# Kernel optimization log

Measured on AMD Instinct MI355X. Metric: run time of the kernel, lower is better.

Reference implementation:

```python
import jax, jax.numpy as jnp
import numpy as np

N_ATOMS = 10000
N_PAIRS = 320000
C = 64        # channel width (pp_nodes[-1], ii_nodes[-1], pi_nodes[-1])
NB = 10       # n_basis
EPS = 1e-3    # torsion-boost epsilon


def setup_inputs() -> dict:
    key = jax.random.key(0)
    ks = jax.random.split(key, 24)
    f32 = jnp.float32

    def w(k, shp):
        return jax.random.normal(k, shp, f32) / np.float32(np.sqrt(shp[0]))

    ind_2 = jax.random.randint(ks[0], (N_PAIRS, 2), 0, N_ATOMS)
    p1 = jax.random.normal(ks[1], (N_ATOMS, C), f32)
    p3 = jax.random.normal(ks[2], (N_ATOMS, 3, C), f32)
    basis = jax.random.uniform(ks[3], (N_PAIRS, NB), dtype=f32)
    d3 = jax.random.normal(ks[4], (N_PAIRS, 3), f32)
    d3 = d3 / jnp.linalg.norm(d3, axis=-1, keepdims=True)  # unit bond directions
    fc_edge = jax.random.uniform(ks[5], (N_PAIRS, 1), dtype=f32)  # cutoff in [0,1]

    return {
        'ind_2': ind_2, 'p1': p1, 'p3': p3, 'basis': basis, 'd3': d3, 'fc_edge': fc_edge,
        'pp_pre_W1': w(ks[6], (C, C)), 'pp_pre_b1': jnp.zeros((C,), f32),
        'pp_pre_W2': w(ks[7], (C, C)), 'pp_pre_b2': jnp.zeros((C,), f32),
        'pi_W': w(ks[8], (2 * C, C * NB)), 'pi_b': jnp.zeros((C * NB,), f32),
        'ii_W': w(ks[9], (C, 2 * C)),
        'pp_post_W1': w(ks[10], (2 * C, C)), 'pp_post_W2': w(ks[11], (C, C)),
        'eq_pp_W': w(ks[12], (C, C)),
        'pp1_W1': w(ks[13], (2 * C, C)), 'pp1_b1': jnp.zeros((C,), f32),
        'pp1_W2': w(ks[14], (C, 2 * C)), 'pp1_b2': jnp.zeros((2 * C,), f32),
    }


def _gc_block(ind_2, p1, p3, basis, d3, fc_edge,
              pp_pre_W1, pp_pre_b1, pp_pre_W2, pp_pre_b2,
              pi_W, pi_b, ii_W, pp_post_W1, pp_post_W2,
              eq_pp_W, pp1_W1, pp1_b1, pp1_W2, pp1_b2):
    n_atoms = p1.shape[0]
    i = ind_2[:, 0]
    j = ind_2[:, 1]

    # ---- InvarLayer ----
    # pp_pre: FF [C,C], tanh, bias
    p1_in = jnp.tanh(jnp.tanh(p1 @ pp_pre_W1 + pp_pre_b1) @ pp_pre_W2 + pp_pre_b2)
    # PILayer: concat(p1[i], p1[j]) -> Dense(C*NB) -> contract with radial basis
    pair = jnp.concatenate([p1_in[i], p1_in[j]], axis=-1)            # (P, 2C)
    h = jnp.tanh(pair @ pi_W + pi_b).reshape(-1, C, NB)              # (P, C, NB)
    i_pair = jnp.einsum('pcb,pb->pc', h, basis)                      # (P, C)
    # ii: FF [2C] (doubled for n_props=2), tanh, no bias
    i_pair = jnp.tanh(i_pair @ ii_W)                                 # (P, 2C)
    # IP: scatter-add onto receiver atom i
    p1_scat = jax.ops.segment_sum(i_pair, i, num_segments=n_atoms)   # (N, 2C)
    # pp_post: FF [C,C], tanh, no bias
    p1_new = jnp.tanh(jnp.tanh(p1_scat @ pp_post_W1) @ pp_post_W2)   # (N, C)

    i1a, i1b = jnp.split(i_pair, 2, axis=-1)  # chunks; rank-3 branch uses i1s[1]

    # ---- torsion boost (compute_torsion_boost_t3) ----
    v = jax.ops.segment_sum(d3 * fc_edge, i, num_segments=n_atoms)   # (N, 3)
    v_i = v[i]
    proj = jnp.sum(v_i * d3, axis=-1, keepdims=True)
    w = v_i - proj * d3                                              # perpendicular part
    w2 = jnp.sum(w * w, axis=-1, keepdims=True)
    g_deg = w2 / (w2 + (10.0 * EPS) ** 2)
    t3 = w * jax.lax.rsqrt(w2 + EPS * EPS) * g_deg                   # (P, 3)
    tb_gate = g_deg * (fc_edge * fc_edge)                            # (P, 1)

    # ---- EquivarLayer ----
    gate = i1b[:, None, :]                                           # (P, 1, C)
    ix = p3[j] * gate + d3[:, :, None] * gate \
         + t3[:, :, None] * (i1b * tb_gate)[:, None, :]              # (P, 3, C)
    p3_new = jax.ops.segment_sum(ix, i, num_segments=n_atoms)        # (N, 3, C)
    p3_new = p3_new @ eq_pp_W                                        # PP: no bias, no act
    dotted = jnp.einsum('ixr,ixr->ir', p3_new, p3_new)               # (N, C)

    # ---- output PP + gating ----
    h2 = jnp.tanh(jnp.concatenate([p1_new, dotted], axis=-1) @ pp1_W1 + pp1_b1)
    h2 = jnp.tanh(h2 @ pp1_W2 + pp1_b2)                              # (N, 2C)
    g1, g3 = jnp.split(h2, 2, axis=-1)
    p1_out = g1                                                      # (N, C)
    p3_out = p3_new * g3[:, None, :]                                 # ScaleLayer
    return p1_out, p3_out


def reference(ind_2, p1, p3, basis, d3, fc_edge,
              pp_pre_W1, pp_pre_b1, pp_pre_W2, pp_pre_b2,
              pi_W, pi_b, ii_W, pp_post_W1, pp_post_W2,
              eq_pp_W, pp1_W1, pp1_b1, pp1_W2, pp1_b2):
    return _gc_block(ind_2, p1, p3, basis, d3, fc_edge,
                     pp_pre_W1, pp_pre_b1, pp_pre_W2, pp_pre_b2,
                     pi_W, pi_b, ii_W, pp_post_W1, pp_post_W2,
                     eq_pp_W, pp1_W1, pp1_b1, pp1_W2, pp1_b2)
```

## Files before the change

kernel.cpp:

```cpp
#include <hip/hip_runtime.h>
#include <hip/hip_bf16.h>

#define N_ATOMS 10000
#define N_PAIRS 320000
#define C_ 64
#define NB_ 10

typedef short bf16x8 __attribute__((ext_vector_type(8)));
typedef float f32x4 __attribute__((ext_vector_type(4)));

__device__ __forceinline__ float bf2f(__hip_bfloat16 x) { return __bfloat162float(x); }
__device__ __forceinline__ float ldf(const void* p, int i, int isf32) {
    return isf32 ? ((const float*)p)[i] : bf2f(((const __hip_bfloat16*)p)[i]);
}
__device__ __forceinline__ short f2bs(float x) {
    __hip_bfloat16 h = __float2bfloat16(x);
    return *reinterpret_cast<short*>(&h);
}
__device__ __forceinline__ float bs2f(unsigned short s) {
    return __uint_as_float(((unsigned)s) << 16);
}
__device__ __forceinline__ float tanh_fast(float x) {
    const float e = __expf(2.0f * x);
    return 1.0f - 2.0f * __builtin_amdgcn_rcpf(e + 1.0f);
}

#define W_PPREW1 0
#define W_PPREB1 4096
#define W_PPREW2 4160
#define W_PPREB2 8256
#define W_PIW    8320
#define W_PIB    90240
#define W_IIW    90880
#define W_PPOSTW1 99072
#define W_PPOSTW2 107264
#define W_EQW    111360
#define W_Q1W    115456
#define W_Q1B    123648
#define W_Q2W    123712
#define W_Q2B    131904
#define W_TOTAL  132032

__device__ __forceinline__ int probe_eval(const void* d3)
{
    float sf = 0.f, sb = 0.f;
    const float* f = (const float*)d3;
    const __hip_bfloat16* b = (const __hip_bfloat16*)d3;
    for (int r = 0; r < 4; r++) {
        float x = f[r*3], y = f[r*3+1], z = f[r*3+2];
        float n = x*x + y*y + z*z;
        sf += isfinite(n) ? fabsf(n - 1.f) : 1e30f;
        float xb = bf2f(b[r*3]), yb = bf2f(b[r*3+1]), zb = bf2f(b[r*3+2]);
        float nb = xb*xb + yb*yb + zb*zb;
        sb += isfinite(nb) ? fabsf(nb - 1.f) : 1e30f;
    }
    return (sf < sb) ? 1 : 0;
}

__global__ __launch_bounds__(256) void k_front(
    const void* __restrict__ d3, const void* __restrict__ fc,
    int* __restrict__ flag, const int* __restrict__ ind2,
    int* __restrict__ cnt, float* __restrict__ v,
    const void* s0, const void* s1, const void* s2, const void* s3,
    const void* s4, const void* s5, const void* s6, const void* s7,
    const void* s8, const void* s9, const void* s10, const void* s11,
    const void* s12, const void* s13,
    float* __restrict__ wbuf)
{
    __shared__ int fsh;
    if (threadIdx.x == 0) {
        const int fv = probe_eval(d3);
        fsh = fv;
        if (blockIdx.x == 0) *flag = fv;
    }
    __syncthreads();
    const int isf32 = fsh;
    if (blockIdx.x < 1250) {
        const int p = blockIdx.x * 256 + threadIdx.x;
        if (p >= N_PAIRS) return;
        const int ia = ind2[2 * p];
        atomicAdd(&cnt[ia], 1);
        const float f = ldf(fc, p, isf32);
        #pragma unroll
        for (int x = 0; x < 3; x++)
            atomicAdd(&v[ia * 3 + x], ldf(d3, 3 * p + x, isf32) * f);
        return;
    }
    const int idx = (blockIdx.x - 1250) * 256 + threadIdx.x;
    if (idx >= W_TOTAL) return;
    const int offw[15] = {W_PPREW1, W_PPREB1, W_PPREW2, W_PPREB2, W_PIW, W_PIB,
                          W_IIW, W_PPOSTW1, W_PPOSTW2, W_EQW, W_Q1W, W_Q1B,
                          W_Q2W, W_Q2B, W_TOTAL};
    const void* srcs[14] = {s0,s1,s2,s3,s4,s5,s6,s7,s8,s9,s10,s11,s12,s13};
    int t = 0;
    while (idx >= offw[t + 1]) t++;
    wbuf[idx] = ldf(srcs[t], idx - offw[t], isf32);
}

__global__ __launch_bounds__(256) void k_scan_wfrag(
    const int* __restrict__ cnt, int* __restrict__ offs, int* __restrict__ cur,
    const float* __restrict__ wbuf,
    short* __restrict__ w1Fh, short* __restrict__ w1Fl,
    short* __restrict__ w2Fh, short* __restrict__ w2Fl,
    short* __restrict__ pAh, short* __restrict__ pAl,
    short* __restrict__ pBh, short* __restrict__ pBl,
    short* __restrict__ pEh, short* __restrict__ pEl,
    short* __restrict__ pQ1h, short* __restrict__ pQ1l,
    short* __restrict__ pQ2h, short* __restrict__ pQ2l)
{
    const int b = blockIdx.x;
    if (b == 0) {
        if (!cnt) return;
        __shared__ int part[256];
        __shared__ int base[257];
        const int t = threadIdx.x;
        const int lo = t * 40, hi = (lo + 40 < N_ATOMS) ? lo + 40 : N_ATOMS;
        int s = 0;
        for (int bb = lo; bb < hi; bb++) s += cnt[bb];
        part[t] = s;
        __syncthreads();
        if (t == 0) {
            int run = 0;
            for (int i = 0; i < 256; i++) { base[i] = run; run += part[i]; }
            base[256] = run;
        }
        __syncthreads();
        int run = base[t];
        for (int bb = lo; bb < hi; bb++) { offs[bb] = run; cur[bb] = run; run += cnt[bb]; }
        if (t == 0) offs[N_ATOMS] = base[256];
        return;
    }
    if (b < 33) {
        const int bb = b - 1;
        const int isW2 = bb >= 16;
        const int idx = (bb - (isW2 ? 16 : 0)) * 256 + threadIdx.x;
        const int j = idx & 7, lane = (idx >> 3) & 63, s2 = (idx >> 9) & 1, ct = idx >> 10;
        const int k = s2 * 32 + (lane >> 4) * 8 + j;
        const int col = ct * 16 + (lane & 15);
        const float wv = wbuf[(isW2 ? W_PPREW2 : W_PPREW1) + k * 64 + col];
        const short hs = f2bs(wv);
        short* dh = isW2 ? w2Fh : w1Fh;
        short* dl = isW2 ? w2Fl : w1Fl;
        dh[idx] = hs;
        dl[idx] = f2bs(wv - bs2f((unsigned short)hs));
        return;
    }
    if (b < 65 || (b >= 97 && b < 129)) {
        const int isQ1 = (b >= 97);
        const int idx = (b - (isQ1 ? 97 : 33)) * 256 + threadIdx.x;
        const int j = idx & 7, lane = (idx >> 3) & 63, s = (idx >> 9) & 3, tt = idx >> 11;
        const int k = s * 32 + (lane >> 4) * 8 + j;
        const int col = tt * 16 + (lane & 15);
        const float wv = wbuf[(isQ1 ? W_Q1W : W_PPOSTW1) + k * 64 + col];
        const short hs = f2bs(wv);
        short* dh = isQ1 ? pQ1h : pAh;
        short* dl = isQ1 ? pQ1l : pAl;
        dh[idx] = hs;
        dl[idx] = f2bs(wv - bs2f((unsigned short)hs));
        return;
    }
    if (b < 97) {
        const int isE = b >= 81;
        const int idx = (b - (isE ? 81 : 65)) * 256 + threadIdx.x;
        const int j = idx & 7, lane = (idx >> 3) & 63, s2 = (idx >> 9) & 1, ct = idx >> 10;
        const int k = s2 * 32 + (lane >> 4) * 8 + j;
        const int col = ct * 16 + (lane & 15);
        const float wv = wbuf[(isE ? W_EQW : W_PPOSTW2) + k * 64 + col];
        const short hs = f2bs(wv);
        short* dh = isE ? pEh : pBh;
        short* dl = isE ? pEl : pBl;
        dh[idx] = hs;
        dl[idx] = f2bs(wv - bs2f((unsigned short)hs));
        return;
    }
    {
        const int idx = (b - 129) * 256 + threadIdx.x;
        const int j = idx & 7, lane = (idx >> 3) & 63, s2 = (idx >> 9) & 1, ct = idx >> 10;
        const int k = s2 * 32 + (lane >> 4) * 8 + j;
        const int col = ct * 16 + (lane & 15);
        const float wv = wbuf[W_Q2W + k * 128 + col];
        const short hs = f2bs(wv);
        pQ2h[idx] = hs;
        pQ2l[idx] = f2bs(wv - bs2f((unsigned short)hs));
    }
}

__global__ __launch_bounds__(256) void k_prep_scatter(
    const float* __restrict__ wbuf,
    short* __restrict__ piWB2,
    short* __restrict__ iiWh, short* __restrict__ iiWl,
    const void* __restrict__ p1, const int* __restrict__ flagp,
    unsigned short* __restrict__ p1h, unsigned short* __restrict__ p1l,
    const int* __restrict__ ind2, int* __restrict__ cur, int* __restrict__ perm,
    const short* __restrict__ w1Fh, const short* __restrict__ w1Fl,
    const short* __restrict__ w2Fh, const short* __restrict__ w2Fl)
{
    __shared__ float hL[64 * 68];
    if (blockIdx.x >= 509) {
        const int p = (blockIdx.x - 509) * 256 + threadIdx.x;
        if (p < N_PAIRS) {
            const int pos = atomicAdd(&cur[ind2[2 * p]], 1);
            perm[pos] = p;
        }
        return;
    }
    if (blockIdx.x < 352) {
        int idx = blockIdx.x * 256 + threadIdx.x;
        if (idx < 81920) {
            const int j = idx & 7, lane = (idx >> 3) & 63, s = (idx >> 9) & 3, T = idx >> 11;
            const int k = s * 32 + (lane >> 4) * 8 + j;
            const int colp = T * 16 + (lane & 15);
            const int b = colp >> 6, c = colp & 63;
            const float v = wbuf[W_PIW + k * 640 + c * 10 + b];
            const short hs = f2bs(v);
            const int cc = idx >> 13, e = idx & 8191;
            piWB2[cc * 16384 + e] = hs;
            piWB2[cc * 16384 + 8192 + e] = f2bs(v - bs2f((unsigned short)hs));
            return;
        }
        idx -= 81920;
        if (idx < 8192) {
            const int j = idx & 7, lane = (idx >> 3) & 63, s2 = (idx >> 9) & 1, ct = idx >> 10;
            const int k = s2 * 32 + (lane >> 4) * 8 + j;
            const int col = ct * 16 + (lane & 15);
            const float wv = wbuf[W_IIW + k * 128 + col];
            const short hs = f2bs(wv);
            iiWh[idx] = hs;
            iiWl[idx] = f2bs(wv - bs2f((unsigned short)hs));
        }
        return;
    }
    const int isf32 = *flagp;
    const int t = threadIdx.x;
    const int lane = t & 63, w = t >> 6, lc = lane & 15, quad = lane >> 4;
    const int B0 = (blockIdx.x - 352) * 64;

    bf16x8 xh[2], xl[2];
    {
        const int a = B0 + w * 16 + lc;
        const int ar = (a < N_ATOMS) ? a : N_ATOMS - 1;
        #pragma unroll
        for (int s2 = 0; s2 < 2; s2++) {
            const int base = ar * 64 + s2 * 32 + quad * 8;
            #pragma unroll
            for (int j = 0; j < 8; j++) {
                const float x = ldf(p1, base + j, isf32);
                const short hs = f2bs(x);
                xh[s2][j] = hs;
                xl[s2][j] = f2bs(x - bs2f((unsigned short)hs));
            }
        }
    }
    #pragma unroll
    for (int tt = 0; tt < 4; tt++) {
        f32x4 acc = {0.f, 0.f, 0.f, 0.f};
        #pragma unroll
        for (int s2 = 0; s2 < 2; s2++) {
            bf16x8 bh = *(const bf16x8*)&w1Fh[((tt * 2 + s2) * 64 + lane) * 8];
            bf16x8 bl = *(const bf16x8*)&w1Fl[((tt * 2 + s2) * 64 + lane) * 8];
            acc = __builtin_amdgcn_mfma_f32_16x16x32_bf16(xh[s2], bh, acc, 0, 0, 0);
            acc = __builtin_amdgcn_mfma_f32_16x16x32_bf16(xl[s2], bh, acc, 0, 0, 0);
            acc = __builtin_amdgcn_mfma_f32_16x16x32_bf16(xh[s2], bl, acc, 0, 0, 0);
        }
        const int c = tt * 16 + lc;
        const float b1v = wbuf[W_PPREB1 + c];
        #pragma unroll
        for (int r = 0; r < 4; r++) {
            const int m = w * 16 + quad * 4 + r;
            hL[m * 68 + c] = tanh_fast(acc[r] + b1v);
        }
    }
    __syncthreads();
    bf16x8 hh[2], hl[2];
    {
        const int row = w * 16 + lc;
        #pragma unroll
        for (int s2 = 0; s2 < 2; s2++) {
            const float* pr = &hL[row * 68 + s2 * 32 + quad * 8];
            #pragma unroll
            for (int j = 0; j < 8; j++) {
                const float x = pr[j];
                const short hs = f2bs(x);
                hh[s2][j] = hs;
                hl[s2][j] = f2bs(x - bs2f((unsigned short)hs));
            }
        }
    }
    #pragma unroll
    for (int tt = 0; tt < 4; tt++) {
        f32x4 acc = {0.f, 0.f, 0.f, 0.f};
        #pragma unroll
        for (int s2 = 0; s2 < 2; s2++) {
            bf16x8 bh = *(const bf16x8*)&w2Fh[((tt * 2 + s2) * 64 + lane) * 8];
            bf16x8 bl = *(const bf16x8*)&w2Fl[((tt * 2 + s2) * 64 + lane) * 8];
            acc = __builtin_amdgcn_mfma_f32_16x16x32_bf16(hh[s2], bh, acc, 0, 0, 0);
            acc = __builtin_amdgcn_mfma_f32_16x16x32_bf16(hl[s2], bh, acc, 0, 0, 0);
            acc = __builtin_amdgcn_mfma_f32_16x16x32_bf16(hh[s2], bl, acc, 0, 0, 0);
        }
        const int c = tt * 16 + lc;
        const float b2v = wbuf[W_PPREB2 + c];
        #pragma unroll
        for (int r = 0; r < 4; r++) {
            const int m = w * 16 + quad * 4 + r;
            const int a = B0 + m;
            if (a < N_ATOMS) {
                const float f = tanh_fast(acc[r] + b2v);
                const short hs = f2bs(f);
                p1h[a * 64 + c] = (unsigned short)hs;
                p1l[a * 64 + c] = (unsigned short)f2bs(f - bs2f((unsigned short)hs));
            }
        }
    }
}

__global__ __launch_bounds__(256) void k_pairs_fused(
    const int* __restrict__ ind2, const void* __restrict__ basis,
    const void* __restrict__ d3, const void* __restrict__ fc,
    const int* __restrict__ perm,
    const void* __restrict__ p3,
    const float* __restrict__ wbuf,
    const short* __restrict__ piWB2,
    const short* __restrict__ iiWh, const short* __restrict__ iiWl,
    const unsigned short* __restrict__ p1h, const unsigned short* __restrict__ p1l,
    const int* __restrict__ flagp, const float* __restrict__ vglob,
    float* __restrict__ p1scat, float* __restrict__ p3acc)
{
    __shared__ __align__(16) char SH[33280];
    __shared__ float basisL[640];
    __shared__ float biasT[640];
    __shared__ int sIL[65], sJL[64];
    __shared__ float d3L[64][3], t3L[64][3], tbL[64];

    unsigned short* Bbuf = (unsigned short*)SH;
    float* preL = (float*)SH;
    float* ipL  = (float*)SH;

    const int t = threadIdx.x;
    const int bid = blockIdx.x;
    const int P0 = ((bid & 7) * 625 + (bid >> 3)) * 64;
    const int isf32 = *flagp;
    const int lane = t & 63;
    const int w = t >> 6;
    const int lc = lane & 15;
    const int quad = lane >> 4;

    if (t < 64) {
        const int p = perm[P0 + t];
        int2 ij = ((const int2*)ind2)[p];
        sIL[t] = ij.x; sJL[t] = ij.y;
        const float vi0 = vglob[ij.x * 3 + 0], vi1 = vglob[ij.x * 3 + 1], vi2 = vglob[ij.x * 3 + 2];
        const float d0 = ldf(d3, 3 * p + 0, isf32);
        const float d1 = ldf(d3, 3 * p + 1, isf32);
        const float d2 = ldf(d3, 3 * p + 2, isf32);
        d3L[t][0] = d0; d3L[t][1] = d1; d3L[t][2] = d2;
        const float proj = vi0 * d0 + vi1 * d1 + vi2 * d2;
        const float w0 = vi0 - proj * d0, w1 = vi1 - proj * d1, w2v = vi2 - proj * d2;
        const float w2 = w0 * w0 + w1 * w1 + w2v * w2v;
        const float g = w2 / (w2 + 1e-4f);
        const float rs = rsqrtf(w2 + 1e-6f);
        t3L[t][0] = w0 * rs * g; t3L[t][1] = w1 * rs * g; t3L[t][2] = w2v * rs * g;
        const float f = ldf(fc, p, isf32);
        tbL[t] = g * f * f;
    }
    if (t == 64) sIL[64] = -1;
    for (int e = t; e < 640; e += 256) {
        const int pm = e / 10, col = e - pm * 10;
        basisL[e] = ldf(basis, perm[P0 + pm] * 10 + col, isf32);
    }
    for (int e = t; e < 640; e += 256) biasT[e] = wbuf[W_PIB + (e & 63) * 10 + (e >> 6)];
    __syncthreads();

    bf16x8 ah[4], al[4];
    {
        const int ia = sIL[w * 16 + lc];
        const int ja = sJL[w * 16 + lc];
        #pragma unroll
        for (int s = 0; s < 4; s++) {
            const int atom = (s < 2) ? ia : ja;
            const int off = atom * 64 + (s & 1) * 32 + quad * 8;
            ah[s] = *(const bf16x8*)(p1h + off);
            al[s] = *(const bf16x8*)(p1l + off);
        }
    }

    float sr[4][4];
    #pragma unroll
    for (int r = 0; r < 4; r++)
        #pragma unroll
        for (int ph = 0; ph < 4; ph++) sr[r][ph] = 0.f;

    for (int cc = 0; cc < 10; cc++) {
        if (cc) __syncthreads();
        {
            const uint4* gsrc = (const uint4*)(piWB2 + cc * 16384);
            uint4* ldst = (uint4*)Bbuf;
            #pragma unroll
            for (int r = 0; r < 8; r++) ldst[r * 256 + t] = gsrc[r * 256 + t];
        }
        __syncthreads();
        #pragma unroll
        for (int tt = 0; tt < 4; tt++) {
            f32x4 acc = {0.f, 0.f, 0.f, 0.f};
            #pragma unroll
            for (int s = 0; s < 4; s++) {
                const int e = ((tt * 4 + s) * 64 + lane) * 8;
                bf16x8 bh = *(const bf16x8*)&Bbuf[e];
                bf16x8 bl = *(const bf16x8*)&Bbuf[8192 + e];
                acc = __builtin_amdgcn_mfma_f32_16x16x32_bf16(ah[s], bh, acc, 0, 0, 0);
                acc = __builtin_amdgcn_mfma_f32_16x16x32_bf16(al[s], bh, acc, 0, 0, 0);
                acc = __builtin_amdgcn_mfma_f32_16x16x32_bf16(ah[s], bl, acc, 0, 0, 0);
            }
            const float bias = biasT[cc * 64 + tt * 16 + lc];
            #pragma unroll
            for (int r = 0; r < 4; r++) {
                const int m = w * 16 + quad * 4 + r;
                const float h = tanh_fast(acc[r] + bias);
                sr[r][tt] += h * basisL[m * 10 + cc];
            }
        }
    }
    __syncthreads();

    #pragma unroll
    for (int r = 0; r < 4; r++)
        #pragma unroll
        for (int ph = 0; ph < 4; ph++)
            preL[(w * 16 + quad * 4 + r) * 68 + ph * 16 + lc] = sr[r][ph];
    __syncthreads();

    bf16x8 ah2[2], al2[2];
    {
        const int row = w * 16 + lc;
        #pragma unroll
        for (int s2 = 0; s2 < 2; s2++) {
            const float* pr2 = &preL[row * 68 + s2 * 32 + quad * 8];
            #pragma unroll
            for (int j = 0; j < 8; j++) {
                const float x = pr2[j];
                const short hs = f2bs(x);
                ah2[s2][j] = hs;
                al2[s2][j] = f2bs(x - bs2f((unsigned short)hs));
            }
        }
    }
    __syncthreads();

    float pv0[16];
    if (t < 192) {
        #pragma unroll
        for (int u = 0; u < 16; u++) pv0[u] = ldf(p3, sJL[u] * 192 + t, isf32);
    }

    #pragma unroll
    for (int ct = 0; ct < 8; ct++) {
        f32x4 acc = {0.f, 0.f, 0.f, 0.f};
        #pragma unroll
        for (int s2 = 0; s2 < 2; s2++) {
            bf16x8 bh = *(const bf16x8*)&iiWh[((ct * 2 + s2) * 64 + lane) * 8];
            bf16x8 bl = *(const bf16x8*)&iiWl[((ct * 2 + s2) * 64 + lane) * 8];
            acc = __builtin_amdgcn_mfma_f32_16x16x32_bf16(ah2[s2], bh, acc, 0, 0, 0);
            acc = __builtin_amdgcn_mfma_f32_16x16x32_bf16(al2[s2], bh, acc, 0, 0, 0);
            acc = __builtin_amdgcn_mfma_f32_16x16x32_bf16(ah2[s2], bl, acc, 0, 0, 0);
        }
        const int ch = ct * 16 + lc;
        #pragma unroll
        for (int r = 0; r < 4; r++) {
            const int m = w * 16 + quad * 4 + r;
            ipL[m * 130 + ch] = tanh_fast(acc[r]);
        }
    }
    __syncthreads();

    if (t < 192) {
        const int x = t >> 6, cc2 = t & 63;
        float acc = 0.f;
        #pragma unroll
        for (int blk = 0; blk < 4; blk++) {
            float pv[16];
            if (blk == 0) {
                #pragma unroll
                for (int u = 0; u < 16; u++) pv[u] = pv0[u];
            } else {
                #pragma unroll
                for (int u = 0; u < 16; u++)
                    pv[u] = ldf(p3, sJL[blk * 16 + u] * 192 + t, isf32);
            }
            #pragma unroll
            for (int u = 0; u < 16; u++) {
                const int m = blk * 16 + u;
                const float ipb = ipL[m * 130 + 64 + cc2];
                acc += (pv[u] + d3L[m][x]) * ipb + t3L[m][x] * (ipb * tbL[m]);
                if (sIL[m + 1] != sIL[m]) {
                    atomicAdd(&p3acc[(size_t)sIL[m] * 192 + t], acc);
                    acc = 0.f;
                }
            }
        }
    } else {
        const int ch0 = t - 192;
        float a0 = 0.f, a1 = 0.f;
        #pragma unroll 8
        for (int m = 0; m < 64; m++) {
            a0 += ipL[m * 130 + ch0];
            a1 += ipL[m * 130 + 64 + ch0];
            if (sIL[m + 1] != sIL[m]) {
                const size_t base = (size_t)sIL[m] * 128;
                atomicAdd(&p1scat[base + ch0], a0);
                atomicAdd(&p1scat[base + 64 + ch0], a1);
                a0 = 0.f; a1 = 0.f;
            }
        }
    }
}

__global__ __launch_bounds__(256) void k_pairs_atomic(
    const int* __restrict__ ind2, const void* __restrict__ basis,
    const void* __restrict__ d3, const void* __restrict__ fc,
    const void* __restrict__ p3,
    const float* __restrict__ wbuf,
    const short* __restrict__ piWB2,
    const short* __restrict__ iiWh, const short* __restrict__ iiWl,
    const unsigned short* __restrict__ p1h, const unsigned short* __restrict__ p1l,
    const int* __restrict__ flagp, const float* __restrict__ vglob,
    float* __restrict__ outA, float* __restrict__ outB)
{
    __shared__ __align__(16) unsigned short Bbuf[8192];
    __shared__ __align__(16) char SH[17408];
    __shared__ float basisL[640];
    __shared__ int sIL[64], sJL[64];
    __shared__ float d3L[64][3], t3L[64][3], tbL[64];

    float* preL = (float*)SH;
    float* i1bL = (float*)SH;

    const int t = threadIdx.x;
    const int P0 = blockIdx.x * 64;
    const int isf32 = *flagp;
    const int lane = t & 63;
    const int w = t >> 6;
    const int lc = lane & 15;
    const int quad = lane >> 4;

    if (t < 64) {
        int2 ij = ((const int2*)ind2)[P0 + t];
        sIL[t] = ij.x; sJL[t] = ij.y;
    }
    for (int e = t; e < 640; e += 256) basisL[e] = ldf(basis, P0 * 10 + e, isf32);
    __syncthreads();

    bf16x8 ah[4], al[4];
    {
        const int ia = sIL[w * 16 + lc];
        const int ja = sJL[w * 16 + lc];
        #pragma unroll
        for (int s = 0; s < 4; s++) {
            const int atom = (s < 2) ? ia : ja;
            const int off = atom * 64 + (s & 1) * 32 + quad * 8;
            ah[s] = *(const bf16x8*)(p1h + off);
            al[s] = *(const bf16x8*)(p1l + off);
        }
    }

    float sr[4][4];
    #pragma unroll
    for (int r = 0; r < 4; r++)
        #pragma unroll
        for (int ph = 0; ph < 4; ph++) sr[r][ph] = 0.f;

    for (int cc = 0; cc < 10; cc++) {
        f32x4 acc[4];
        #pragma unroll
        for (int tt = 0; tt < 4; tt++) acc[tt] = (f32x4){0.f, 0.f, 0.f, 0.f};

        __syncthreads();
        {
            const uint4* gsrc = (const uint4*)(piWB2 + cc * 16384);
            uint4* ldst = (uint4*)Bbuf;
            #pragma unroll
            for (int r = 0; r < 4; r++) ldst[r * 256 + t] = gsrc[r * 256 + t];
        }
        __syncthreads();
        #pragma unroll
        for (int tt = 0; tt < 4; tt++) {
            #pragma unroll
            for (int s = 0; s < 4; s++) {
                bf16x8 bfr = *(const bf16x8*)&Bbuf[((tt * 4 + s) * 64 + lane) * 8];
                acc[tt] = __builtin_amdgcn_mfma_f32_16x16x32_bf16(ah[s], bfr, acc[tt], 0, 0, 0);
                acc[tt] = __builtin_amdgcn_mfma_f32_16x16x32_bf16(al[s], bfr, acc[tt], 0, 0, 0);
            }
        }
        __syncthreads();
        {
            const uint4* gsrc = (const uint4*)(piWB2 + cc * 16384 + 8192);
            uint4* ldst = (uint4*)Bbuf;
            #pragma unroll
            for (int r = 0; r < 4; r++) ldst[r * 256 + t] = gsrc[r * 256 + t];
        }
        __syncthreads();
        #pragma unroll
        for (int tt = 0; tt < 4; tt++) {
            #pragma unroll
            for (int s = 0; s < 4; s++) {
                bf16x8 bfr = *(const bf16x8*)&Bbuf[((tt * 4 + s) * 64 + lane) * 8];
                acc[tt] = __builtin_amdgcn_mfma_f32_16x16x32_bf16(ah[s], bfr, acc[tt], 0, 0, 0);
            }
            const int c = tt * 16 + lc;
            const float bias = wbuf[W_PIB + c * 10 + cc];
            #pragma unroll
            for (int r = 0; r < 4; r++) {
                const int m = w * 16 + quad * 4 + r;
                const float h = tanh_fast(acc[tt][r] + bias);
                sr[r][tt] += h * basisL[m * 10 + cc];
            }
        }
    }

    #pragma unroll
    for (int r = 0; r < 4; r++)
        #pragma unroll
        for (int ph = 0; ph < 4; ph++)
            preL[(w * 16 + quad * 4 + r) * 68 + ph * 16 + lc] = sr[r][ph];
    __syncthreads();

    bf16x8 ah2[2], al2[2];
    {
        const int row = w * 16 + lc;
        #pragma unroll
        for (int s2 = 0; s2 < 2; s2++) {
            const float* pr2 = &preL[row * 68 + s2 * 32 + quad * 8];
            #pragma unroll
            for (int j = 0; j < 8; j++) {
                const float x = pr2[j];
                const short hs = f2bs(x);
                ah2[s2][j] = hs;
                al2[s2][j] = f2bs(x - bs2f((unsigned short)hs));
            }
        }
    }
    __syncthreads();

    #pragma unroll
    for (int ct = 0; ct < 8; ct++) {
        f32x4 acc = {0.f, 0.f, 0.f, 0.f};
        #pragma unroll
        for (int s2 = 0; s2 < 2; s2++) {
            bf16x8 bh = *(const bf16x8*)&iiWh[((ct * 2 + s2) * 64 + lane) * 8];
            bf16x8 bl = *(const bf16x8*)&iiWl[((ct * 2 + s2) * 64 + lane) * 8];
            acc = __builtin_amdgcn_mfma_f32_16x16x32_bf16(ah2[s2], bh, acc, 0, 0, 0);
            acc = __builtin_amdgcn_mfma_f32_16x16x32_bf16(al2[s2], bh, acc, 0, 0, 0);
            acc = __builtin_amdgcn_mfma_f32_16x16x32_bf16(ah2[s2], bl, acc, 0, 0, 0);
        }
        const int ch = ct * 16 + lc;
        #pragma unroll
        for (int r = 0; r < 4; r++) {
            const int m = w * 16 + quad * 4 + r;
            const float val = tanh_fast(acc[r]);
            atomicAdd(&outA[(size_t)sIL[m] * 128 + ch], val);
            if (ch >= 64) i1bL[m * 64 + (ch - 64)] = val;
        }
    }

    __syncthreads();
    if (t < 64) {
        const int m = t;
        const int ia = sIL[m];
        const float vi0 = vglob[ia * 3 + 0], vi1 = vglob[ia * 3 + 1], vi2 = vglob[ia * 3 + 2];
        const float d0 = ldf(d3, (P0 + m) * 3 + 0, isf32);
        const float d1 = ldf(d3, (P0 + m) * 3 + 1, isf32);
        const float d2 = ldf(d3, (P0 + m) * 3 + 2, isf32);
        d3L[m][0] = d0; d3L[m][1] = d1; d3L[m][2] = d2;
        const float proj = vi0 * d0 + vi1 * d1 + vi2 * d2;
        const float w0 = vi0 - proj * d0, w1 = vi1 - proj * d1, w2v = vi2 - proj * d2;
        const float w2 = w0 * w0 + w1 * w1 + w2v * w2v;
        const float g = w2 / (w2 + 1e-4f);
        const float rs = rsqrtf(w2 + 1e-6f);
        t3L[m][0] = w0 * rs * g; t3L[m][1] = w1 * rs * g; t3L[m][2] = w2v * rs * g;
        const float f = ldf(fc, P0 + m, isf32);
        tbL[m] = g * f * f;
    }
    __syncthreads();
    const int c = lane;
    #pragma unroll 4
    for (int mm = 0; mm < 16; mm++) {
        const int m = w * 16 + mm;
        const float bv = i1bL[m * 64 + c];
        const float coef = bv * tbL[m];
        #pragma unroll
        for (int x = 0; x < 3; x++) {
            const float p3v = ldf(p3, sJL[m] * 192 + x * 64 + c, isf32);
            atomicAdd(&outB[(size_t)sIL[m] * 192 + x * 64 + c],
                      p3v * bv + d3L[m][x] * bv + t3L[m][x] * coef);
        }
    }
}

__global__ __launch_bounds__(256) void k_final_mfma(
    const float* __restrict__ p1scat, const float* __restrict__ p3acc,
    const float* __restrict__ wbuf, const int* __restrict__ flagp,
    const short* __restrict__ pAh, const short* __restrict__ pAl,
    const short* __restrict__ pBh, const short* __restrict__ pBl,
    const short* __restrict__ pEh, const short* __restrict__ pEl,
    const short* __restrict__ pQ1h, const short* __restrict__ pQ1l,
    const short* __restrict__ pQ2h, const short* __restrict__ pQ2l,
    void* __restrict__ out)
{
    __shared__ float hL[64 * 68];
    __shared__ float catL[64 * 132];
    const int isf32 = *flagp;
    const int t = threadIdx.x;
    const int lane = t & 63, w = t >> 6, lc = lane & 15, quad = lane >> 4;
    const int B0 = blockIdx.x * 64;
    const int arow = B0 + w * 16 + lc;
    const int ar = (arow < N_ATOMS) ? arow : N_ATOMS - 1;

    {
        bf16x8 xh[4], xl[4];
        #pragma unroll
        for (int s = 0; s < 4; s++) {
            const float* src = p1scat + (size_t)ar * 128 + s * 32 + quad * 8;
            #pragma unroll
            for (int j = 0; j < 8; j++) {
                const float x = src[j];
                const short hs = f2bs(x);
                xh[s][j] = hs;
                xl[s][j] = f2bs(x - bs2f((unsigned short)hs));
            }
        }
        #pragma unroll
        for (int tt = 0; tt < 4; tt++) {
            f32x4 acc = {0.f, 0.f, 0.f, 0.f};
            #pragma unroll
            for (int s = 0; s < 4; s++) {
                bf16x8 bh = *(const bf16x8*)&pAh[((tt * 4 + s) * 64 + lane) * 8];
                bf16x8 bl = *(const bf16x8*)&pAl[((tt * 4 + s) * 64 + lane) * 8];
                acc = __builtin_amdgcn_mfma_f32_16x16x32_bf16(xh[s], bh, acc, 0, 0, 0);
                acc = __builtin_amdgcn_mfma_f32_16x16x32_bf16(xl[s], bh, acc, 0, 0, 0);
                acc = __builtin_amdgcn_mfma_f32_16x16x32_bf16(xh[s], bl, acc, 0, 0, 0);
            }
            const int c = tt * 16 + lc;
            #pragma unroll
            for (int r = 0; r < 4; r++)
                hL[(w * 16 + quad * 4 + r) * 68 + c] = tanh_fast(acc[r]);
        }
    }
    __syncthreads();

    {
        bf16x8 hh[2], hl[2];
        const int row = w * 16 + lc;
        #pragma unroll
        for (int s2 = 0; s2 < 2; s2++) {
            const float* pr = &hL[row * 68 + s2 * 32 + quad * 8];
            #pragma unroll
            for (int j = 0; j < 8; j++) {
                const float x = pr[j];
                const short hs = f2bs(x);
                hh[s2][j] = hs;
                hl[s2][j] = f2bs(x - bs2f((unsigned short)hs));
            }
        }
        #pragma unroll
        for (int tt = 0; tt < 4; tt++) {
            f32x4 acc = {0.f, 0.f, 0.f, 0.f};
            #pragma unroll
            for (int s2 = 0; s2 < 2; s2++) {
                bf16x8 bh = *(const bf16x8*)&pBh[((tt * 2 + s2) * 64 + lane) * 8];
                bf16x8 bl = *(const bf16x8*)&pBl[((tt * 2 + s2) * 64 + lane) * 8];
                acc = __builtin_amdgcn_mfma_f32_16x16x32_bf16(hh[s2], bh, acc, 0, 0, 0);
                acc = __builtin_amdgcn_mfma_f32_16x16x32_bf16(hl[s2], bh, acc, 0, 0, 0);
                acc = __builtin_amdgcn_mfma_f32_16x16x32_bf16(hh[s2], bl, acc, 0, 0, 0);
            }
            const int c = tt * 16 + lc;
            #pragma unroll
            for (int r = 0; r < 4; r++)
                catL[(w * 16 + quad * 4 + r) * 132 + c] = tanh_fast(acc[r]);
        }
    }

    float pn[3][4][4];
    #pragma unroll
    for (int x = 0; x < 3; x++) {
        bf16x8 ph[2], pl[2];
        #pragma unroll
        for (int s2 = 0; s2 < 2; s2++) {
            const float* src = p3acc + (size_t)ar * 192 + x * 64 + s2 * 32 + quad * 8;
            #pragma unroll
            for (int j = 0; j < 8; j++) {
                const float xv = src[j];
                const short hs = f2bs(xv);
                ph[s2][j] = hs;
                pl[s2][j] = f2bs(xv - bs2f((unsigned short)hs));
            }
        }
        #pragma unroll
        for (int tt = 0; tt < 4; tt++) {
            f32x4 acc = {0.f, 0.f, 0.f, 0.f};
            #pragma unroll
            for (int s2 = 0; s2 < 2; s2++) {
                bf16x8 bh = *(const bf16x8*)&pEh[((tt * 2 + s2) * 64 + lane) * 8];
                bf16x8 bl = *(const bf16x8*)&pEl[((tt * 2 + s2) * 64 + lane) * 8];
                acc = __builtin_amdgcn_mfma_f32_16x16x32_bf16(ph[s2], bh, acc, 0, 0, 0);
                acc = __builtin_amdgcn_mfma_f32_16x16x32_bf16(pl[s2], bh, acc, 0, 0, 0);
                acc = __builtin_amdgcn_mfma_f32_16x16x32_bf16(ph[s2], bl, acc, 0, 0, 0);
            }
            #pragma unroll
            for (int r = 0; r < 4; r++) pn[x][tt][r] = acc[r];
        }
    }
    #pragma unroll
    for (int tt = 0; tt < 4; tt++) {
        const int c = tt * 16 + lc;
        #pragma unroll
        for (int r = 0; r < 4; r++) {
            const float d = pn[0][tt][r] * pn[0][tt][r]
                          + pn[1][tt][r] * pn[1][tt][r]
                          + pn[2][tt][r] * pn[2][tt][r];
            catL[(w * 16 + quad * 4 + r) * 132 + 64 + c] = d;
        }
    }
    __syncthreads();

    {
        bf16x8 ch[4], cl[4];
        const int row = w * 16 + lc;
        #pragma unroll
        for (int s = 0; s < 4; s++) {
            const float* pr = &catL[row * 132 + s * 32 + quad * 8];
            #pragma unroll
            for (int j = 0; j < 8; j++) {
                const float x = pr[j];
                const short hs = f2bs(x);
                ch[s][j] = hs;
                cl[s][j] = f2bs(x - bs2f((unsigned short)hs));
            }
        }
        #pragma unroll
        for (int tt = 0; tt < 4; tt++) {
            f32x4 acc = {0.f, 0.f, 0.f, 0.f};
            #pragma unroll
            for (int s = 0; s < 4; s++) {
                bf16x8 bh = *(const bf16x8*)&pQ1h[((tt * 4 + s) * 64 + lane) * 8];
                bf16x8 bl = *(const bf16x8*)&pQ1l[((tt * 4 + s) * 64 + lane) * 8];
                acc = __builtin_amdgcn_mfma_f32_16x16x32_bf16(ch[s], bh, acc, 0, 0, 0);
                acc = __builtin_amdgcn_mfma_f32_16x16x32_bf16(cl[s], bh, acc, 0, 0, 0);
                acc = __builtin_amdgcn_mfma_f32_16x16x32_bf16(ch[s], bl, acc, 0, 0, 0);
            }
            const int c = tt * 16 + lc;
            const float b1v = wbuf[W_Q1B + c];
            #pragma unroll
            for (int r = 0; r < 4; r++)
                hL[(w * 16 + quad * 4 + r) * 68 + c] = tanh_fast(acc[r] + b1v);
        }
    }
    __syncthreads();

    bf16x8 gh[2], gl[2];
    {
        const int row = w * 16 + lc;
        #pragma unroll
        for (int s2 = 0; s2 < 2; s2++) {
            const float* pr = &hL[row * 68 + s2 * 32 + quad * 8];
            #pragma unroll
            for (int j = 0; j < 8; j++) {
                const float x = pr[j];
                const short hs = f2bs(x);
                gh[s2][j] = hs;
                gl[s2][j] = f2bs(x - bs2f((unsigned short)hs));
            }
        }
    }
    float* p1o32 = (float*)out;
    float* p3o32 = p1o32 + 640000;
    __hip_bfloat16* p1o16 = (__hip_bfloat16*)out;
    __hip_bfloat16* p3o16 = p1o16 + 640000;
    #pragma unroll
    for (int ct = 0; ct < 8; ct++) {
        f32x4 acc = {0.f, 0.f, 0.f, 0.f};
        #pragma unroll
        for (int s2 = 0; s2 < 2; s2++) {
            bf16x8 bh = *(const bf16x8*)&pQ2h[((ct * 2 + s2) * 64 + lane) * 8];
            bf16x8 bl = *(const bf16x8*)&pQ2l[((ct * 2 + s2) * 64 + lane) * 8];
            acc = __builtin_amdgcn_mfma_f32_16x16x32_bf16(gh[s2], bh, acc, 0, 0, 0);
            acc = __builtin_amdgcn_mfma_f32_16x16x32_bf16(gl[s2], bh, acc, 0, 0, 0);
            acc = __builtin_amdgcn_mfma_f32_16x16x32_bf16(gh[s2], bl, acc, 0, 0, 0);
        }
        const int col = ct * 16 + lc;
        const float qb = wbuf[W_Q2B + col];
        #pragma unroll
        for (int r = 0; r < 4; r++) {
            const int m = w * 16 + quad * 4 + r;
            const int a = B0 + m;
            if (a >= N_ATOMS) continue;
            const float val = tanh_fast(acc[r] + qb);
            if (ct < 4) {
                if (isf32) p1o32[a * 64 + col] = val;
                else       p1o16[a * 64 + col] = __float2bfloat16(val);
            } else {
                const int c2 = col - 64;
                #pragma unroll
                for (int x = 0; x < 3; x++) {
                    const float pv = pn[x][ct - 4][r] * val;
                    if (isf32) p3o32[a * 192 + x * 64 + c2] = pv;
                    else       p3o16[a * 192 + x * 64 + c2] = __float2bfloat16(pv);
                }
            }
        }
    }
}

extern "C" void kernel_launch(void* const* d_in, const int* in_sizes, int n_in,
                              void* d_out, int out_size, void* d_ws, size_t ws_size,
                              hipStream_t stream)
{
    const int* ind2 = (const int*)d_in[0];
    const void* p1    = d_in[1];
    const void* p3    = d_in[2];
    const void* basis = d_in[3];
    const void* d3    = d_in[4];
    const void* fc    = d_in[5];

    char* W = (char*)d_ws;
    float* wbuf  = (float*)(W + 0);
    short* piWB2 = (short*)(W + 528128);
    short* iiWh  = (short*)(W + 1183488);
    short* iiWl  = (short*)(W + 1199872);
    unsigned short* p1h = (unsigned short*)(W + 1216256);
    unsigned short* p1l = (unsigned short*)(W + 2496256);
    int* flag = (int*)(W + 3776256);
    short* w1Fh = (short*)(W + 3776320);
    short* w1Fl = (short*)(W + 3784512);
    short* w2Fh = (short*)(W + 3792704);
    short* w2Fl = (short*)(W + 3800896);
    short* pAh  = (short*)(W + 3809088);
    short* pAl  = (short*)(W + 3825472);
    short* pBh  = (short*)(W + 3841856);
    short* pBl  = (short*)(W + 3850048);
    short* pEh  = (short*)(W + 3858240);
    short* pEl  = (short*)(W + 3866432);
    short* pQ1h = (short*)(W + 3874624);
    short* pQ1l = (short*)(W + 3891008);
    short* pQ2h = (short*)(W + 3907392);
    short* pQ2l = (short*)(W + 3923776);

    const int fused = (ws_size >= 18260224ULL) ? 1 : 0;

    if (fused) {
        int* offs     = (int*)(W + 3940160);
        int* cur      = (int*)(W + 3980224);
        int* perm     = (int*)(W + 4020224);
        int* cnt      = (int*)(W + 5300224);
        float* v      = (float*)(W + 5340224);
        float* p1scat = (float*)(W + 5460224);
        float* p3acc  = (float*)(W + 10580224);

        hipMemsetAsync(cnt, 0, 40000 + 120000 + 5120000 + 7680000, stream);
        k_front<<<1766, 256, 0, stream>>>(d3, fc, flag, ind2, cnt, v,
            d_in[6], d_in[7], d_in[8], d_in[9], d_in[10], d_in[11], d_in[12],
            d_in[13], d_in[14], d_in[15], d_in[16], d_in[17], d_in[18], d_in[19],
            wbuf);
        k_scan_wfrag<<<161, 256, 0, stream>>>(cnt, offs, cur, wbuf,
                                              w1Fh, w1Fl, w2Fh, w2Fl,
                                              pAh, pAl, pBh, pBl, pEh, pEl,
                                              pQ1h, pQ1l, pQ2h, pQ2l);
        k_prep_scatter<<<1759, 256, 0, stream>>>(wbuf, piWB2, iiWh, iiWl, p1, flag,
                                                 p1h, p1l, ind2, cur, perm,
                                                 w1Fh, w1Fl, w2Fh, w2Fl);
        k_pairs_fused<<<5000, 256, 0, stream>>>(ind2, basis, d3, fc, perm, p3,
                                                wbuf, piWB2, iiWh, iiWl,
                                                p1h, p1l, flag, v, p1scat, p3acc);
        k_final_mfma<<<157, 256, 0, stream>>>(p1scat, p3acc, wbuf, flag,
                                              pAh, pAl, pBh, pBl, pEh, pEl,
                                              pQ1h, pQ1l, pQ2h, pQ2l, d_out);
    } else {
        int* cnt      = (int*)(W + 3940160);
        float* v      = (float*)(W + 3980160);
        float* p1scat = (float*)(W + 4100160);
        float* p3acc  = (float*)(W + 9220160);

        hipMemsetAsync(cnt, 0, 40000 + 120000 + 5120000 + 7680000, stream);
        k_front<<<1766, 256, 0, stream>>>(d3, fc, flag, ind2, cnt, v,
            d_in[6], d_in[7], d_in[8], d_in[9], d_in[10], d_in[11], d_in[12],
            d_in[13], d_in[14], d_in[15], d_in[16], d_in[17], d_in[18], d_in[19],
            wbuf);
        k_scan_wfrag<<<161, 256, 0, stream>>>(nullptr, nullptr, nullptr, wbuf,
                                              w1Fh, w1Fl, w2Fh, w2Fl,
                                              pAh, pAl, pBh, pBl, pEh, pEl,
                                              pQ1h, pQ1l, pQ2h, pQ2l);
        k_prep_scatter<<<509, 256, 0, stream>>>(wbuf, piWB2, iiWh, iiWl, p1, flag,
                                                p1h, p1l, nullptr, nullptr, nullptr,
                                                w1Fh, w1Fl, w2Fh, w2Fl);
        k_pairs_atomic<<<5000, 256, 0, stream>>>(ind2, basis, d3, fc, p3,
                                                 wbuf, piWB2, iiWh, iiWl,
                                                 p1h, p1l, flag, v,
                                                 p1scat, p3acc);
        k_final_mfma<<<157, 256, 0, stream>>>(p1scat, p3acc, wbuf, flag,
                                              pAh, pAl, pBh, pBl, pEh, pEl,
                                              pQ1h, pQ1l, pQ2h, pQ2l, d_out);
    }
}
```

Baseline: 484.9 us.

## Record per-pair rank during counting and fold weight fragment prep into front kernel

The counting pass now saves the atomicAdd return value as a per-pair rank, so the counting-sort scatter writes perm[offs[ia]+rank[p]] directly instead of running a second round of atomics on a cursor array. All weight-fragment conversions (pi, ii, pre, post, eq, output weights) move into the front kernel and read the raw inputs directly, so they no longer wait for the wbuf copy. A tiny single-block scan kernel replaces the scan that was mixed into the weight-fragment kernel. This adds a rank buffer (more workspace, higher fused threshold) and makes the sorted order within each atom depend on atomic ordering rather than being stable.

```diff
diff --git a/kernel.cpp b/kernel.cpp
--- a/kernel.cpp
+++ b/kernel.cpp
@@ -57,49 +57,22 @@
     return (sf < sb) ? 1 : 0;
 }
 
+__global__ void k_probe(const void* __restrict__ d3, int* __restrict__ flag)
+{
+    if (threadIdx.x == 0 && blockIdx.x == 0) *flag = probe_eval(d3);
+}
+
 __global__ __launch_bounds__(256) void k_front(
     const void* __restrict__ d3, const void* __restrict__ fc,
     int* __restrict__ flag, const int* __restrict__ ind2,
-    int* __restrict__ cnt, float* __restrict__ v,
+    int* __restrict__ cnt, float* __restrict__ v, int* __restrict__ rank,
     const void* s0, const void* s1, const void* s2, const void* s3,
     const void* s4, const void* s5, const void* s6, const void* s7,
     const void* s8, const void* s9, const void* s10, const void* s11,
     const void* s12, const void* s13,
-    float* __restrict__ wbuf)
-{
-    __shared__ int fsh;
-    if (threadIdx.x == 0) {
-        const int fv = probe_eval(d3);
-        fsh = fv;
-        if (blockIdx.x == 0) *flag = fv;
-    }
-    __syncthreads();
-    const int isf32 = fsh;
-    if (blockIdx.x < 1250) {
-        const int p = blockIdx.x * 256 + threadIdx.x;
-        if (p >= N_PAIRS) return;
-        const int ia = ind2[2 * p];
-        atomicAdd(&cnt[ia], 1);
-        const float f = ldf(fc, p, isf32);
-        #pragma unroll
-        for (int x = 0; x < 3; x++)
-            atomicAdd(&v[ia * 3 + x], ldf(d3, 3 * p + x, isf32) * f);
-        return;
-    }
-    const int idx = (blockIdx.x - 1250) * 256 + threadIdx.x;
-    if (idx >= W_TOTAL) return;
-    const int offw[15] = {W_PPREW1, W_PPREB1, W_PPREW2, W_PPREB2, W_PIW, W_PIB,
-                          W_IIW, W_PPOSTW1, W_PPOSTW2, W_EQW, W_Q1W, W_Q1B,
-                          W_Q2W, W_Q2B, W_TOTAL};
-    const void* srcs[14] = {s0,s1,s2,s3,s4,s5,s6,s7,s8,s9,s10,s11,s12,s13};
-    int t = 0;
-    while (idx >= offw[t + 1]) t++;
-    wbuf[idx] = ldf(srcs[t], idx - offw[t], isf32);
-}
-
-__global__ __launch_bounds__(256) void k_scan_wfrag(
-    const int* __restrict__ cnt, int* __restrict__ offs, int* __restrict__ cur,
-    const float* __restrict__ wbuf,
+    float* __restrict__ wbuf,
+    short* __restrict__ piWB2,
+    short* __restrict__ iiWh, short* __restrict__ iiWl,
     short* __restrict__ w1Fh, short* __restrict__ w1Fl,
     short* __restrict__ w2Fh, short* __restrict__ w2Fl,
     short* __restrict__ pAh, short* __restrict__ pAl,
@@ -108,36 +81,73 @@
     short* __restrict__ pQ1h, short* __restrict__ pQ1l,
     short* __restrict__ pQ2h, short* __restrict__ pQ2l)
 {
+    __shared__ int fsh;
+    if (threadIdx.x == 0) {
+        const int fv = probe_eval(d3);
+        fsh = fv;
+        if (blockIdx.x == 0) *flag = fv;
+    }
+    __syncthreads();
+    const int isf32 = fsh;
     const int b = blockIdx.x;
-    if (b == 0) {
-        if (!cnt) return;
-        __shared__ int part[256];
-        __shared__ int base[257];
-        const int t = threadIdx.x;
-        const int lo = t * 40, hi = (lo + 40 < N_ATOMS) ? lo + 40 : N_ATOMS;
-        int s = 0;
-        for (int bb = lo; bb < hi; bb++) s += cnt[bb];
-        part[t] = s;
-        __syncthreads();
-        if (t == 0) {
-            int run = 0;
-            for (int i = 0; i < 256; i++) { base[i] = run; run += part[i]; }
-            base[256] = run;
-        }
-        __syncthreads();
-        int run = base[t];
-        for (int bb = lo; bb < hi; bb++) { offs[bb] = run; cur[bb] = run; run += cnt[bb]; }
-        if (t == 0) offs[N_ATOMS] = base[256];
+    const int t = threadIdx.x;
+
+    if (b < 1250) {
+        const int p = b * 256 + t;
+        if (p >= N_PAIRS) return;
+        const int ia = ind2[2 * p];
+        rank[p] = atomicAdd(&cnt[ia], 1);
+        const float f = ldf(fc, p, isf32);
+        #pragma unroll
+        for (int x = 0; x < 3; x++)
+            atomicAdd(&v[ia * 3 + x], ldf(d3, 3 * p + x, isf32) * f);
         return;
     }
-    if (b < 33) {
-        const int bb = b - 1;
-        const int isW2 = bb >= 16;
-        const int idx = (bb - (isW2 ? 16 : 0)) * 256 + threadIdx.x;
-        const int j = idx & 7, lane = (idx >> 3) & 63, s2 = (idx >> 9) & 1, ct = idx >> 10;
-        const int k = s2 * 32 + (lane >> 4) * 8 + j;
+    if (b < 1766) {
+        const int idx = (b - 1250) * 256 + t;
+        if (idx >= W_TOTAL) return;
+        const int offw[15] = {W_PPREW1, W_PPREB1, W_PPREW2, W_PPREB2, W_PIW, W_PIB,
+                              W_IIW, W_PPOSTW1, W_PPOSTW2, W_EQW, W_Q1W, W_Q1B,
+                              W_Q2W, W_Q2B, W_TOTAL};
+        const void* srcs[14] = {s0,s1,s2,s3,s4,s5,s6,s7,s8,s9,s10,s11,s12,s13};
+        int q = 0;
+        while (idx >= offw[q + 1]) q++;
+        wbuf[idx] = ldf(srcs[q], idx - offw[q], isf32);
+        return;
+    }
+    if (b < 2086) {
+        const int idx = (b - 1766) * 256 + t;
+        const int j = idx & 7, lane = (idx >> 3) & 63, sgrp = (idx >> 9) & 3, T = idx >> 11;
+        const int k = sgrp * 32 + (lane >> 4) * 8 + j;
+        const int colp = T * 16 + (lane & 15);
+        const int bb = colp >> 6, c = colp & 63;
+        const float wv = ldf(s4, k * 640 + c * 10 + bb, isf32);
+        const short hs = f2bs(wv);
+        const int cc = idx >> 13, e = idx & 8191;
+        piWB2[cc * 16384 + e] = hs;
+        piWB2[cc * 16384 + 8192 + e] = f2bs(wv - bs2f((unsigned short)hs));
+        return;
+    }
+    if (b < 2118) {
+        const int idx = (b - 2086) * 256 + t;
+        const int j = idx & 7, lane = (idx >> 3) & 63, sgrp = (idx >> 9) & 1, ct = idx >> 10;
+        const int k = sgrp * 32 + (lane >> 4) * 8 + j;
         const int col = ct * 16 + (lane & 15);
-        const float wv = wbuf[(isW2 ? W_PPREW2 : W_PPREW1) + k * 64 + col];
+        const float wv = ldf(s6, k * 128 + col, isf32);
+        const short hs = f2bs(wv);
+        iiWh[idx] = hs;
+        iiWl[idx] = f2bs(wv - bs2f((unsigned short)hs));
+        return;
+    }
+    if (b < 2150) {
+        const int local = b - 2118;
+        const int isW2 = local >= 16;
+        const int idx = (local - (isW2 ? 16 : 0)) * 256 + t;
+        const int j = idx & 7, lane = (idx >> 3) & 63, sgrp = (idx >> 9) & 1, ct = idx >> 10;
+        const int k = sgrp * 32 + (lane >> 4) * 8 + j;
+        const int col = ct * 16 + (lane & 15);
+        const void* srcw = isW2 ? s2 : s0;
+        const float wv = ldf(srcw, k * 64 + col, isf32);
         const short hs = f2bs(wv);
         short* dh = isW2 ? w2Fh : w1Fh;
         short* dl = isW2 ? w2Fl : w1Fl;
@@ -145,13 +155,14 @@
         dl[idx] = f2bs(wv - bs2f((unsigned short)hs));
         return;
     }
-    if (b < 65 || (b >= 97 && b < 129)) {
-        const int isQ1 = (b >= 97);
-        const int idx = (b - (isQ1 ? 97 : 33)) * 256 + threadIdx.x;
-        const int j = idx & 7, lane = (idx >> 3) & 63, s = (idx >> 9) & 3, tt = idx >> 11;
-        const int k = s * 32 + (lane >> 4) * 8 + j;
+    if (b < 2182 || (b >= 2214 && b < 2246)) {
+        const int isQ1 = (b >= 2214);
+        const int idx = (b - (isQ1 ? 2214 : 2150)) * 256 + t;
+        const int j = idx & 7, lane = (idx >> 3) & 63, sgrp = (idx >> 9) & 3, tt = idx >> 11;
+        const int k = sgrp * 32 + (lane >> 4) * 8 + j;
         const int col = tt * 16 + (lane & 15);
-        const float wv = wbuf[(isQ1 ? W_Q1W : W_PPOSTW1) + k * 64 + col];
+        const void* srcw = isQ1 ? s10 : s7;
+        const float wv = ldf(srcw, k * 64 + col, isf32);
         const short hs = f2bs(wv);
         short* dh = isQ1 ? pQ1h : pAh;
         short* dl = isQ1 ? pQ1l : pAl;
@@ -159,13 +170,14 @@
         dl[idx] = f2bs(wv - bs2f((unsigned short)hs));
         return;
     }
-    if (b < 97) {
-        const int isE = b >= 81;
-        const int idx = (b - (isE ? 81 : 65)) * 256 + threadIdx.x;
-        const int j = idx & 7, lane = (idx >> 3) & 63, s2 = (idx >> 9) & 1, ct = idx >> 10;
-        const int k = s2 * 32 + (lane >> 4) * 8 + j;
+    if (b < 2214) {
+        const int isE = b >= 2198;
+        const int idx = (b - (isE ? 2198 : 2182)) * 256 + t;
+        const int j = idx & 7, lane = (idx >> 3) & 63, sgrp = (idx >> 9) & 1, ct = idx >> 10;
+        const int k = sgrp * 32 + (lane >> 4) * 8 + j;
         const int col = ct * 16 + (lane & 15);
-        const float wv = wbuf[(isE ? W_EQW : W_PPOSTW2) + k * 64 + col];
+        const void* srcw = isE ? s9 : s8;
+        const float wv = ldf(srcw, k * 64 + col, isf32);
         const short hs = f2bs(wv);
         short* dh = isE ? pEh : pBh;
         short* dl = isE ? pEl : pBl;
@@ -174,66 +186,61 @@
         return;
     }
     {
-        const int idx = (b - 129) * 256 + threadIdx.x;
-        const int j = idx & 7, lane = (idx >> 3) & 63, s2 = (idx >> 9) & 1, ct = idx >> 10;
-        const int k = s2 * 32 + (lane >> 4) * 8 + j;
+        const int idx = (b - 2246) * 256 + t;
+        const int j = idx & 7, lane = (idx >> 3) & 63, sgrp = (idx >> 9) & 1, ct = idx >> 10;
+        const int k = sgrp * 32 + (lane >> 4) * 8 + j;
         const int col = ct * 16 + (lane & 15);
-        const float wv = wbuf[W_Q2W + k * 128 + col];
+        const float wv = ldf(s12, k * 128 + col, isf32);
         const short hs = f2bs(wv);
         pQ2h[idx] = hs;
         pQ2l[idx] = f2bs(wv - bs2f((unsigned short)hs));
     }
 }
 
+__global__ __launch_bounds__(256) void k_scan(const int* __restrict__ cnt,
+                                              int* __restrict__ offs)
+{
+    __shared__ int part[256];
+    __shared__ int base[257];
+    const int t = threadIdx.x;
+    const int lo = t * 40, hi = (lo + 40 < N_ATOMS) ? lo + 40 : N_ATOMS;
+    int s = 0;
+    for (int b = lo; b < hi; b++) s += cnt[b];
+    part[t] = s;
+    __syncthreads();
+    if (t == 0) {
+        int run = 0;
+        for (int i = 0; i < 256; i++) { base[i] = run; run += part[i]; }
+        base[256] = run;
+    }
+    __syncthreads();
+    int run = base[t];
+    for (int b = lo; b < hi; b++) { offs[b] = run; run += cnt[b]; }
+    if (t == 0) offs[N_ATOMS] = base[256];
+}
+
 __global__ __launch_bounds__(256) void k_prep_scatter(
     const float* __restrict__ wbuf,
-    short* __restrict__ piWB2,
-    short* __restrict__ iiWh, short* __restrict__ iiWl,
     const void* __restrict__ p1, const int* __restrict__ flagp,
     unsigned short* __restrict__ p1h, unsigned short* __restrict__ p1l,
-    const int* __restrict__ ind2, int* __restrict__ cur, int* __restrict__ perm,
+    const int* __restrict__ ind2, const int* __restrict__ offs,
+    const int* __restrict__ rank, int* __restrict__ perm,
     const short* __restrict__ w1Fh, const short* __restrict__ w1Fl,
     const short* __restrict__ w2Fh, const short* __restrict__ w2Fl)
 {
     __shared__ float hL[64 * 68];
-    if (blockIdx.x >= 509) {
-        const int p = (blockIdx.x - 509) * 256 + threadIdx.x;
+    if (blockIdx.x >= 157) {
+        const int p = (blockIdx.x - 157) * 256 + threadIdx.x;
         if (p < N_PAIRS) {
-            const int pos = atomicAdd(&cur[ind2[2 * p]], 1);
-            perm[pos] = p;
-        }
-        return;
-    }
-    if (blockIdx.x < 352) {
-        int idx = blockIdx.x * 256 + threadIdx.x;
-        if (idx < 81920) {
-            const int j = idx & 7, lane = (idx >> 3) & 63, s = (idx >> 9) & 3, T = idx >> 11;
-            const int k = s * 32 + (lane >> 4) * 8 + j;
-            const int colp = T * 16 + (lane & 15);
-            const int b = colp >> 6, c = colp & 63;
-            const float v = wbuf[W_PIW + k * 640 + c * 10 + b];
-            const short hs = f2bs(v);
-            const int cc = idx >> 13, e = idx & 8191;
-            piWB2[cc * 16384 + e] = hs;
-            piWB2[cc * 16384 + 8192 + e] = f2bs(v - bs2f((unsigned short)hs));
-            return;
-        }
-        idx -= 81920;
-        if (idx < 8192) {
-            const int j = idx & 7, lane = (idx >> 3) & 63, s2 = (idx >> 9) & 1, ct = idx >> 10;
-            const int k = s2 * 32 + (lane >> 4) * 8 + j;
-            const int col = ct * 16 + (lane & 15);
-            const float wv = wbuf[W_IIW + k * 128 + col];
-            const short hs = f2bs(wv);
-            iiWh[idx] = hs;
-            iiWl[idx] = f2bs(wv - bs2f((unsigned short)hs));
+            const int ia = ind2[2 * p];
+            perm[offs[ia] + rank[p]] = p;
         }
         return;
     }
     const int isf32 = *flagp;
     const int t = threadIdx.x;
     const int lane = t & 63, w = t >> 6, lc = lane & 15, quad = lane >> 4;
-    const int B0 = (blockIdx.x - 352) * 64;
+    const int B0 = blockIdx.x * 64;
 
     bf16x8 xh[2], xl[2];
     {
@@ -942,28 +949,26 @@
     short* pQ2h = (short*)(W + 3907392);
     short* pQ2l = (short*)(W + 3923776);
 
-    const int fused = (ws_size >= 18260224ULL) ? 1 : 0;
+    const int fused = (ws_size >= 19500224ULL) ? 1 : 0;
 
     if (fused) {
         int* offs     = (int*)(W + 3940160);
-        int* cur      = (int*)(W + 3980224);
-        int* perm     = (int*)(W + 4020224);
-        int* cnt      = (int*)(W + 5300224);
-        float* v      = (float*)(W + 5340224);
-        float* p1scat = (float*)(W + 5460224);
-        float* p3acc  = (float*)(W + 10580224);
+        int* rank     = (int*)(W + 3980224);
+        int* perm     = (int*)(W + 5260224);
+        int* cnt      = (int*)(W + 6540224);
+        float* v      = (float*)(W + 6580224);
+        float* p1scat = (float*)(W + 6700224);
+        float* p3acc  = (float*)(W + 11820224);
 
         hipMemsetAsync(cnt, 0, 40000 + 120000 + 5120000 + 7680000, stream);
-        k_front<<<1766, 256, 0, stream>>>(d3, fc, flag, ind2, cnt, v,
+        k_front<<<2278, 256, 0, stream>>>(d3, fc, flag, ind2, cnt, v, rank,
             d_in[6], d_in[7], d_in[8], d_in[9], d_in[10], d_in[11], d_in[12],
             d_in[13], d_in[14], d_in[15], d_in[16], d_in[17], d_in[18], d_in[19],
-            wbuf);
-        k_scan_wfrag<<<161, 256, 0, stream>>>(cnt, offs, cur, wbuf,
-                                              w1Fh, w1Fl, w2Fh, w2Fl,
-                                              pAh, pAl, pBh, pBl, pEh, pEl,
-                                              pQ1h, pQ1l, pQ2h, pQ2l);
-        k_prep_scatter<<<1759, 256, 0, stream>>>(wbuf, piWB2, iiWh, iiWl, p1, flag,
-                                                 p1h, p1l, ind2, cur, perm,
+            wbuf, piWB2, iiWh, iiWl, w1Fh, w1Fl, w2Fh, w2Fl,
+            pAh, pAl, pBh, pBl, pEh, pEl, pQ1h, pQ1l, pQ2h, pQ2l);
+        k_scan<<<1, 256, 0, stream>>>(cnt, offs);
+        k_prep_scatter<<<1407, 256, 0, stream>>>(wbuf, p1, flag, p1h, p1l,
+                                                 ind2, offs, rank, perm,
                                                  w1Fh, w1Fl, w2Fh, w2Fl);
         k_pairs_fused<<<5000, 256, 0, stream>>>(ind2, basis, d3, fc, perm, p3,
                                                 wbuf, piWB2, iiWh, iiWl,
@@ -976,18 +981,16 @@
         float* v      = (float*)(W + 3980160);
         float* p1scat = (float*)(W + 4100160);
         float* p3acc  = (float*)(W + 9220160);
+        int* rank     = (int*)(W + 16900160);
 
         hipMemsetAsync(cnt, 0, 40000 + 120000 + 5120000 + 7680000, stream);
-        k_front<<<1766, 256, 0, stream>>>(d3, fc, flag, ind2, cnt, v,
+        k_front<<<2278, 256, 0, stream>>>(d3, fc, flag, ind2, cnt, v, rank,
             d_in[6], d_in[7], d_in[8], d_in[9], d_in[10], d_in[11], d_in[12],
             d_in[13], d_in[14], d_in[15], d_in[16], d_in[17], d_in[18], d_in[19],
-            wbuf);
-        k_scan_wfrag<<<161, 256, 0, stream>>>(nullptr, nullptr, nullptr, wbuf,
-                                              w1Fh, w1Fl, w2Fh, w2Fl,
-                                              pAh, pAl, pBh, pBl, pEh, pEl,
-                                              pQ1h, pQ1l, pQ2h, pQ2l);
-        k_prep_scatter<<<509, 256, 0, stream>>>(wbuf, piWB2, iiWh, iiWl, p1, flag,
-                                                p1h, p1l, nullptr, nullptr, nullptr,
+            wbuf, piWB2, iiWh, iiWl, w1Fh, w1Fl, w2Fh, w2Fl,
+            pAh, pAl, pBh, pBl, pEh, pEl, pQ1h, pQ1l, pQ2h, pQ2l);
+        k_prep_scatter<<<157, 256, 0, stream>>>(wbuf, p1, flag, p1h, p1l,
+                                                nullptr, nullptr, nullptr, nullptr,
                                                 w1Fh, w1Fl, w2Fh, w2Fl);
         k_pairs_atomic<<<5000, 256, 0, stream>>>(ind2, basis, d3, fc, p3,
                                                  wbuf, piWB2, iiWh, iiWl,
```

After: 458.7 us. -5.4%, faster.
